# Kernel optimization log

Measured on AMD Instinct MI355X. Metric: run time of the kernel, lower is better.

## Reference

```python
import jax, jax.numpy as jnp
import numpy as np


def setup_inputs() -> dict:
    key = jax.random.key(0)
    k1, k2 = jax.random.split(key)
    B, D, S = 8, 64, 512
    x = jax.random.normal(k1, (B, D, S), dtype=jnp.float32)
    # bracket_products[0]: bias-free Linear(2*D -> D); stored as (2*D, D), applied feat @ W
    W = jax.random.normal(k2, (2 * D, D), dtype=jnp.float32) * (1.0 / np.sqrt(2 * D))
    return {"x": x, "W": W}


def reference(x, W):
    # x: (B, D, S); W: (2D, D)
    B, D, S = x.shape
    # torch builds y_out[b, :, i, j] = concat(x[b,:,j], x[b,:,i]) for i >= j (tril), zeros elsewhere,
    # then applies Linear(2D->D). Split W so the full linear is a broadcast sum of two per-position
    # projections, avoiding the explicit (B, 2D, S, S) scatter.
    W_w, W_h = W[:D], W[D:]                      # x_w part (col j), x_h part (row i)
    a = jnp.einsum('bdj,dk->bjk', x, W_w)        # (B, S, D): column-j contribution
    b = jnp.einsum('bdi,dk->bik', x, W_h)        # (B, S, D): row-i contribution
    mask = jnp.tril(jnp.ones((S, S), dtype=x.dtype))  # rows i >= cols j
    # pair[b,i,j,k] == bracket linear output at (row i, col j); zero on strict upper triangle
    pair = (a[:, None, :, :] + b[:, :, None, :]) * mask[None, :, :, None]  # (B, S, S, D)
    n = jnp.linalg.norm(pair, axis=-1)           # L2 over channel dim -> (B, S, S)
    wmat = 1.0 - n                                # upper triangle: 1 - 0 = 1, matching torch
    # torch: einsum('bdw,bdwi->bdi', x, weight) with weight (B,1,S,S) broadcast over d
    c = jnp.einsum('bdw,bwi->bdi', x, wmat)       # contract over row index w
    return c
```

## Files before the change

kernel.cpp:

```cpp
#include <hip/hip_runtime.h>
#include <hip/hip_bf16.h>
#include <math.h>

#define NB 8
#define ND 64
#define NS 512

typedef __attribute__((ext_vector_type(8))) short bf16x8;
typedef __attribute__((ext_vector_type(4))) float f32x4;
typedef __attribute__((ext_vector_type(4))) unsigned int u32x4;
typedef __attribute__((ext_vector_type(2))) unsigned int u32x2;

__device__ __forceinline__ unsigned int pk2(float lo, float hi) {
    __hip_bfloat162 h = __float22bfloat162_rn(make_float2(lo, hi));
    unsigned int u;
    __builtin_memcpy(&u, &h, 4);
    return u;
}
__device__ __forceinline__ unsigned short f2bf_s(float f) {
    __hip_bfloat16 h = __float2bfloat16(f);
    unsigned short u;
    __builtin_memcpy(&u, &h, 2);
    return u;
}

#define MFMA __builtin_amdgcn_mfma_f32_16x16x32_bf16

__global__ __launch_bounds__(256) void k_warm(const float* __restrict__ x,
                                              const float* __restrict__ W) {
    int idx = blockIdx.x * 256 + threadIdx.x;
    float4 v = ((const float4*)x)[idx];
    float s = v.x + v.y + v.z + v.w;
    if (idx < 2048) {
        float4 w4 = ((const float4*)W)[idx];
        s += w4.x + w4.y + w4.z + w4.w;
    }
    asm volatile("" :: "v"(s));
}

__global__ __launch_bounds__(256, 2) void k_part(const float* __restrict__ x,
                                                 const float* __restrict__ W,
                                                 float* __restrict__ part) {
    __shared__ __align__(16) unsigned short WT[128 * 64];
    __shared__ __align__(16) unsigned short xwd_i[64 * 64];
    __shared__ __align__(16) unsigned short xwd_u[64 * 64];
    __shared__ __align__(16) unsigned short xdw[64 * 64];
    __shared__ __align__(16) unsigned short alds[64 * 64];
    __shared__ __align__(16) unsigned short blds[64 * 64];
    __shared__ __align__(16) unsigned short wmb[64 * 64];
    __shared__ float na_lds[64], nb_lds[64];

    int b = blockIdx.y;
    int v = blockIdx.x;
    int u = 0;
    while ((u + 1) * (u + 2) / 2 <= v) ++u;
    int ti = v - u * (u + 1) / 2;
    int i0 = ti * 64, w0 = u * 64;

    int t = threadIdx.x;
    int lane = t & 63, wv = t >> 6, c = lane & 15, g = lane >> 4, c7 = c & 7;
    int wl = t & 63, w2 = t >> 6;

    float xi_[16], xu_[16];
#pragma unroll
    for (int j = 0; j < 2; ++j)
#pragma unroll
        for (int e = 0; e < 8; ++e) {
            int d = 8 * (2 * w2 + j) + e;
            const float* base = x + ((size_t)(b * ND) + d) * NS;
            xi_[8 * j + e] = base[i0 + wl];
            xu_[8 * j + e] = base[w0 + wl];
        }
    float4 xd_[4];
#pragma unroll
    for (int q = 0; q < 2; ++q) {
        int e = t + 256 * q;
        int d = e >> 3, wc = e & 7;
        const float4* p4 = (const float4*)(x + ((size_t)(b * ND) + d) * NS + w0 + 8 * wc);
        xd_[2 * q]     = p4[0];
        xd_[2 * q + 1] = p4[1];
    }
#pragma unroll
    for (int j = 0; j < 2; ++j) {
        int dblk = 2 * w2 + j;
        u32x4 hi, hu;
#pragma unroll
        for (int e = 0; e < 4; ++e) {
            hi[e] = pk2(xi_[8 * j + 2 * e], xi_[8 * j + 2 * e + 1]);
            hu[e] = pk2(xu_[8 * j + 2 * e], xu_[8 * j + 2 * e + 1]);
        }
        *(u32x4*)&xwd_i[wl * 64 + ((dblk ^ (wl & 7)) << 3)] = hi;
        *(u32x4*)&xwd_u[wl * 64 + ((dblk ^ (wl & 7)) << 3)] = hu;
    }
#pragma unroll
    for (int q = 0; q < 2; ++q) {
        int e = t + 256 * q;
        int d = e >> 3, wc = e & 7;
        float4 v0 = xd_[2 * q], v1 = xd_[2 * q + 1];
        u32x4 h;
        h[0] = pk2(v0.x, v0.y); h[1] = pk2(v0.z, v0.w);
        h[2] = pk2(v1.x, v1.y); h[3] = pk2(v1.z, v1.w);
        *(u32x4*)&xdw[d * 64 + ((wc ^ (d & 7)) << 3)] = h;
    }
    {
        int n = t & 127, half = t >> 7;
        float wv_[32];
#pragma unroll
        for (int p = 0; p < 4; ++p)
#pragma unroll
            for (int dd = 0; dd < 8; ++dd) {
                int dg = half * 4 + p;
                wv_[8 * p + dd] =
                    W[(size_t)(dg * 8 + dd) * ND + (n & 63) + ((n >> 6) * (ND * ND))];
            }
#pragma unroll
        for (int p = 0; p < 4; ++p) {
            int dg = half * 4 + p;
            u32x4 h;
#pragma unroll
            for (int dd = 0; dd < 4; ++dd)
                h[dd] = pk2(wv_[8 * p + 2 * dd], wv_[8 * p + 2 * dd + 1]);
            *(u32x4*)&WT[n * 64 + ((dg ^ (n & 7)) << 3)] = h;
        }
    }
    __syncthreads();

    {
        f32x4 aacc[4] = {{0,0,0,0},{0,0,0,0},{0,0,0,0},{0,0,0,0}};
        f32x4 bacc[4] = {{0,0,0,0},{0,0,0,0},{0,0,0,0},{0,0,0,0}};
#pragma unroll
        for (int ks = 0; ks < 2; ++ks) {
            int row = 16 * wv + c;
            bf16x8 Pi = *(const bf16x8*)&xwd_i[row * 64 + (((4 * ks + g) ^ c7) << 3)];
            bf16x8 Pu = *(const bf16x8*)&xwd_u[row * 64 + (((4 * ks + g) ^ c7) << 3)];
#pragma unroll
            for (int qb = 0; qb < 4; ++qb) {
                bf16x8 Qw = *(const bf16x8*)&WT[(16 * qb + c) * 64 + (((4 * ks + g) ^ c7) << 3)];
                bf16x8 Qh = *(const bf16x8*)&WT[(64 + 16 * qb + c) * 64 + (((4 * ks + g) ^ c7) << 3)];
                aacc[qb] = MFMA(Pi, Qw, aacc[qb], 0, 0, 0);
                bacc[qb] = MFMA(Pu, Qh, bacc[qb], 0, 0, 0);
            }
        }
#pragma unroll
        for (int r = 0; r < 4; ++r) {
            float sa = aacc[0][r] * aacc[0][r] + aacc[1][r] * aacc[1][r]
                     + aacc[2][r] * aacc[2][r] + aacc[3][r] * aacc[3][r];
            float sb = bacc[0][r] * bacc[0][r] + bacc[1][r] * bacc[1][r]
                     + bacc[2][r] * bacc[2][r] + bacc[3][r] * bacc[3][r];
            sa += __shfl_xor(sa, 1, 64); sa += __shfl_xor(sa, 2, 64);
            sa += __shfl_xor(sa, 4, 64); sa += __shfl_xor(sa, 8, 64);
            sb += __shfl_xor(sb, 1, 64); sb += __shfl_xor(sb, 2, 64);
            sb += __shfl_xor(sb, 4, 64); sb += __shfl_xor(sb, 8, 64);
            if (c == 0) {
                na_lds[16 * wv + 4 * g + r] = sa;
                nb_lds[16 * wv + 4 * g + r] = sb;
            }
        }
#pragma unroll
        for (int qb = 0; qb < 4; ++qb)
#pragma unroll
            for (int r = 0; r < 4; ++r) {
                int row = 16 * wv + 4 * g + r, k = 16 * qb + c;
                int off = row * 64 + (((k >> 3) ^ (row & 7)) << 3) + (k & 7);
                alds[off] = f2bf_s(aacc[qb][r]);
                blds[off] = f2bf_s(bacc[qb][r]);
            }
    }
    __syncthreads();

    {
        int wrow = 16 * wv + c;
        bf16x8 P0 = *(const bf16x8*)&blds[wrow * 64 + ((g ^ c7) << 3)];
        bf16x8 P1 = *(const bf16x8*)&blds[wrow * 64 + (((4 + g) ^ c7) << 3)];
        float nbv[4];
#pragma unroll
        for (int r = 0; r < 4; ++r) nbv[r] = nb_lds[16 * wv + 4 * g + r];
        int wbase = w0 + 16 * wv + 4 * g;
#pragma unroll
        for (int n = 0; n < 4; ++n) {
            int arow = 16 * n + c;
            f32x4 a1 = {0.f, 0.f, 0.f, 0.f};
            bf16x8 Q0 = *(const bf16x8*)&alds[arow * 64 + ((g ^ c7) << 3)];
            bf16x8 Q1 = *(const bf16x8*)&alds[arow * 64 + (((4 + g) ^ c7) << 3)];
            a1 = MFMA(P0, Q0, a1, 0, 0, 0);
            a1 = MFMA(P1, Q1, a1, 0, 0, 0);
            float navv = na_lds[arow];
            int i_glob = i0 + arow;
            float vals[4];
#pragma unroll
            for (int r = 0; r < 4; ++r) {
                float s2v = navv + nbv[r] + 2.f * a1[r];
                vals[r] = (i_glob <= wbase + r) ? -sqrtf(fmaxf(s2v, 0.f)) : 0.f;
            }
            u32x2 pk;
            pk[0] = pk2(vals[0], vals[1]);
            pk[1] = pk2(vals[2], vals[3]);
            int wblk = 2 * wv + (g >> 1);
            *(u32x2*)&wmb[arow * 64 + ((wblk ^ (arow & 7)) << 3) + 4 * (g & 1)] = pk;
        }
    }
    __syncthreads();

    {
        int il = 16 * wv + c;
        bf16x8 a20 = *(const bf16x8*)&wmb[il * 64 + ((g ^ c7) << 3)];
        bf16x8 a21 = *(const bf16x8*)&wmb[il * 64 + (((4 + g) ^ c7) << 3)];
#pragma unroll
        for (int nd = 0; nd < 4; ++nd) {
            int d = 16 * nd + c;
            bf16x8 q0 = *(const bf16x8*)&xdw[d * 64 + ((g ^ c7) << 3)];
            bf16x8 q1 = *(const bf16x8*)&xdw[d * 64 + (((4 + g) ^ c7) << 3)];
            f32x4 acc = {0.f, 0.f, 0.f, 0.f};
            acc = MFMA(a20, q0, acc, 0, 0, 0);
            acc = MFMA(a21, q1, acc, 0, 0, 0);
            float* pp = part + (((size_t)u * NB + b) * ND + d) * NS + i0 + 16 * wv + 4 * g;
            *(f32x4*)pp = acc;
        }
    }
}

__global__ __launch_bounds__(128) void k_red(const float* __restrict__ x,
                                             const float* __restrict__ part,
                                             float* __restrict__ out) {
    __shared__ float red[2];
    int b = blockIdx.y, d = blockIdx.x, t = threadIdx.x;
    const float* xr = x + ((size_t)b * ND + d) * NS;

    float4 xv = *(const float4*)(xr + 4 * t);
    float s = xv.x + xv.y + xv.z + xv.w;
#pragma unroll
    for (int m = 32; m >= 1; m >>= 1) s += __shfl_xor(s, m, 64);
    if ((t & 63) == 0) red[t >> 6] = s;
    __syncthreads();
    float rs = red[0] + red[1];

    int it = t >> 4;
    f32x4 vv = {rs, rs, rs, rs};
#pragma unroll
    for (int u = 0; u < 8; ++u) {
        if (u >= it) {
            f32x4 pv = *(const f32x4*)&part[(((size_t)u * NB + b) * ND + d) * NS + 4 * t];
            vv[0] += pv[0]; vv[1] += pv[1]; vv[2] += pv[2]; vv[3] += pv[3];
        }
    }
    *(f32x4*)&out[((size_t)b * ND + d) * NS + 4 * t] = vv;
}

extern "C" void kernel_launch(void* const* d_in, const int* in_sizes, int n_in,
                              void* d_out, int out_size, void* d_ws, size_t ws_size,
                              hipStream_t stream) {
    const float* x = (const float*)d_in[0];
    const float* W = (const float*)d_in[1];
    float* out  = (float*)d_out;
    float* part = (float*)d_ws;

    k_warm<<<dim3(256),    dim3(256), 0, stream>>>(x, W);
    k_part<<<dim3(36, NB), dim3(256), 0, stream>>>(x, W, part);
    k_red <<<dim3(ND, NB), dim3(128), 0, stream>>>(x, part, out);
}
```

Before: 22.19 us.

## Precompute per-position projections and norms in a prep kernel, drop redundant recompute

The tile kernel recomputed the a and b projections (x times W) for both its row and column blocks in every one of 36 tiles per batch. A separate prep kernel now computes each 64-position block's projections, squared norms and a bf16 copy of x once, writing them to the workspace. The pair kernel then just loads bf16 fragments directly from global memory into registers. The warm-up kernel is removed. This trades redundant MFMA work and W staging for extra global round-trips and one more kernel-launch dependency.

```diff
diff --git a/kernel.cpp b/kernel.cpp
--- a/kernel.cpp
+++ b/kernel.cpp
@@ -8,8 +8,8 @@
 
 typedef __attribute__((ext_vector_type(8))) short bf16x8;
 typedef __attribute__((ext_vector_type(4))) float f32x4;
+typedef __attribute__((ext_vector_type(4))) unsigned short us4;
 typedef __attribute__((ext_vector_type(4))) unsigned int u32x4;
-typedef __attribute__((ext_vector_type(2))) unsigned int u32x2;
 
 __device__ __forceinline__ unsigned int pk2(float lo, float hi) {
     __hip_bfloat162 h = __float22bfloat162_rn(make_float2(lo, hi));
@@ -26,29 +26,120 @@
 
 #define MFMA __builtin_amdgcn_mfma_f32_16x16x32_bf16
 
-__global__ __launch_bounds__(256) void k_warm(const float* __restrict__ x,
-                                              const float* __restrict__ W) {
-    int idx = blockIdx.x * 256 + threadIdx.x;
-    float4 v = ((const float4*)x)[idx];
-    float s = v.x + v.y + v.z + v.w;
-    if (idx < 2048) {
-        float4 w4 = ((const float4*)W)[idx];
-        s += w4.x + w4.y + w4.z + w4.w;
-    }
-    asm volatile("" :: "v"(s));
-}
-
-__global__ __launch_bounds__(256, 2) void k_part(const float* __restrict__ x,
-                                                 const float* __restrict__ W,
-                                                 float* __restrict__ part) {
+__global__ __launch_bounds__(256) void k_prep(const float* __restrict__ x,
+                                              const float* __restrict__ W,
+                                              unsigned short* __restrict__ a_bf,
+                                              unsigned short* __restrict__ b_bf,
+                                              float* __restrict__ na,
+                                              float* __restrict__ nb,
+                                              unsigned short* __restrict__ x_bf) {
+    __shared__ __align__(16) unsigned short xT[64 * 64];
     __shared__ __align__(16) unsigned short WT[128 * 64];
-    __shared__ __align__(16) unsigned short xwd_i[64 * 64];
-    __shared__ __align__(16) unsigned short xwd_u[64 * 64];
-    __shared__ __align__(16) unsigned short xdw[64 * 64];
-    __shared__ __align__(16) unsigned short alds[64 * 64];
-    __shared__ __align__(16) unsigned short blds[64 * 64];
-    __shared__ __align__(16) unsigned short wmb[64 * 64];
-    __shared__ float na_lds[64], nb_lds[64];
+
+    int b  = blockIdx.y;
+    int j0 = blockIdx.x * 64;
+    int t  = threadIdx.x;
+    int lane = t & 63, wv = t >> 6, c = lane & 15, g = lane >> 4, c7 = c & 7;
+    int wl = t & 63, w2 = t >> 6;
+
+    float xi_[16];
+#pragma unroll
+    for (int j = 0; j < 2; ++j)
+#pragma unroll
+        for (int e = 0; e < 8; ++e) {
+            int d = 8 * (2 * w2 + j) + e;
+            xi_[8 * j + e] = x[((size_t)(b * ND) + d) * NS + j0 + wl];
+        }
+#pragma unroll
+    for (int j = 0; j < 2; ++j) {
+        int dblk = 2 * w2 + j;
+        u32x4 h;
+#pragma unroll
+        for (int e = 0; e < 4; ++e)
+            h[e] = pk2(xi_[8 * j + 2 * e], xi_[8 * j + 2 * e + 1]);
+        *(u32x4*)&xT[wl * 64 + ((dblk ^ (wl & 7)) << 3)] = h;
+    }
+    {
+        int n = t & 127, half = t >> 7;
+        float wv_[32];
+#pragma unroll
+        for (int p = 0; p < 4; ++p)
+#pragma unroll
+            for (int dd = 0; dd < 8; ++dd) {
+                int dg = half * 4 + p;
+                wv_[8 * p + dd] =
+                    W[(size_t)(dg * 8 + dd) * ND + (n & 63) + ((n >> 6) * (ND * ND))];
+            }
+#pragma unroll
+        for (int p = 0; p < 4; ++p) {
+            int dg = half * 4 + p;
+            u32x4 h;
+#pragma unroll
+            for (int dd = 0; dd < 4; ++dd)
+                h[dd] = pk2(wv_[8 * p + 2 * dd], wv_[8 * p + 2 * dd + 1]);
+            *(u32x4*)&WT[n * 64 + ((dg ^ (n & 7)) << 3)] = h;
+        }
+    }
+#pragma unroll
+    for (int q = 0; q < 2; ++q) {
+        int e = t + 256 * q;
+        int d = e >> 3, wc = e & 7;
+        const float4* p4 = (const float4*)(x + ((size_t)(b * ND) + d) * NS + j0 + 8 * wc);
+        float4 v0 = p4[0], v1 = p4[1];
+        u32x4 h;
+        h[0] = pk2(v0.x, v0.y); h[1] = pk2(v0.z, v0.w);
+        h[2] = pk2(v1.x, v1.y); h[3] = pk2(v1.z, v1.w);
+        *(u32x4*)(x_bf + ((size_t)(b * ND) + d) * NS + j0 + 8 * wc) = h;
+    }
+    __syncthreads();
+
+    f32x4 aacc[4] = {{0,0,0,0},{0,0,0,0},{0,0,0,0},{0,0,0,0}};
+    f32x4 bacc[4] = {{0,0,0,0},{0,0,0,0},{0,0,0,0},{0,0,0,0}};
+#pragma unroll
+    for (int ks = 0; ks < 2; ++ks) {
+        int row = 16 * wv + c;
+        bf16x8 P = *(const bf16x8*)&xT[row * 64 + (((4 * ks + g) ^ c7) << 3)];
+#pragma unroll
+        for (int qb = 0; qb < 4; ++qb) {
+            bf16x8 Qw = *(const bf16x8*)&WT[(16 * qb + c) * 64 + (((4 * ks + g) ^ c7) << 3)];
+            bf16x8 Qh = *(const bf16x8*)&WT[(64 + 16 * qb + c) * 64 + (((4 * ks + g) ^ c7) << 3)];
+            aacc[qb] = MFMA(P, Qw, aacc[qb], 0, 0, 0);
+            bacc[qb] = MFMA(P, Qh, bacc[qb], 0, 0, 0);
+        }
+    }
+#pragma unroll
+    for (int r = 0; r < 4; ++r) {
+        float sa = aacc[0][r] * aacc[0][r] + aacc[1][r] * aacc[1][r]
+                 + aacc[2][r] * aacc[2][r] + aacc[3][r] * aacc[3][r];
+        float sb = bacc[0][r] * bacc[0][r] + bacc[1][r] * bacc[1][r]
+                 + bacc[2][r] * bacc[2][r] + bacc[3][r] * bacc[3][r];
+        sa += __shfl_xor(sa, 1, 64); sa += __shfl_xor(sa, 2, 64);
+        sa += __shfl_xor(sa, 4, 64); sa += __shfl_xor(sa, 8, 64);
+        sb += __shfl_xor(sb, 1, 64); sb += __shfl_xor(sb, 2, 64);
+        sb += __shfl_xor(sb, 4, 64); sb += __shfl_xor(sb, 8, 64);
+        if (c == 0) {
+            na[b * NS + j0 + 16 * wv + 4 * g + r] = sa;
+            nb[b * NS + j0 + 16 * wv + 4 * g + r] = sb;
+        }
+    }
+#pragma unroll
+    for (int qb = 0; qb < 4; ++qb)
+#pragma unroll
+        for (int r = 0; r < 4; ++r) {
+            int row = 16 * wv + 4 * g + r, k = 16 * qb + c;
+            size_t off = ((size_t)b * NS + j0 + row) * ND + k;
+            a_bf[off] = f2bf_s(aacc[qb][r]);
+            b_bf[off] = f2bf_s(bacc[qb][r]);
+        }
+}
+
+__global__ __launch_bounds__(256) void k_c(const unsigned short* __restrict__ x_bf,
+                                           const unsigned short* __restrict__ a_bf,
+                                           const unsigned short* __restrict__ b_bf,
+                                           const float* __restrict__ na,
+                                           const float* __restrict__ nb,
+                                           float* __restrict__ part) {
+    __shared__ unsigned short wm_lds[64 * 64];
 
     int b = blockIdx.y;
     int v = blockIdx.x;
@@ -58,164 +149,71 @@
     int i0 = ti * 64, w0 = u * 64;
 
     int t = threadIdx.x;
-    int lane = t & 63, wv = t >> 6, c = lane & 15, g = lane >> 4, c7 = c & 7;
-    int wl = t & 63, w2 = t >> 6;
-
-    float xi_[16], xu_[16];
-#pragma unroll
-    for (int j = 0; j < 2; ++j)
-#pragma unroll
-        for (int e = 0; e < 8; ++e) {
-            int d = 8 * (2 * w2 + j) + e;
-            const float* base = x + ((size_t)(b * ND) + d) * NS;
-            xi_[8 * j + e] = base[i0 + wl];
-            xu_[8 * j + e] = base[w0 + wl];
-        }
-    float4 xd_[4];
-#pragma unroll
-    for (int q = 0; q < 2; ++q) {
-        int e = t + 256 * q;
-        int d = e >> 3, wc = e & 7;
-        const float4* p4 = (const float4*)(x + ((size_t)(b * ND) + d) * NS + w0 + 8 * wc);
-        xd_[2 * q]     = p4[0];
-        xd_[2 * q + 1] = p4[1];
-    }
-#pragma unroll
-    for (int j = 0; j < 2; ++j) {
-        int dblk = 2 * w2 + j;
-        u32x4 hi, hu;
-#pragma unroll
-        for (int e = 0; e < 4; ++e) {
-            hi[e] = pk2(xi_[8 * j + 2 * e], xi_[8 * j + 2 * e + 1]);
-            hu[e] = pk2(xu_[8 * j + 2 * e], xu_[8 * j + 2 * e + 1]);
-        }
-        *(u32x4*)&xwd_i[wl * 64 + ((dblk ^ (wl & 7)) << 3)] = hi;
-        *(u32x4*)&xwd_u[wl * 64 + ((dblk ^ (wl & 7)) << 3)] = hu;
-    }
-#pragma unroll
-    for (int q = 0; q < 2; ++q) {
-        int e = t + 256 * q;
-        int d = e >> 3, wc = e & 7;
-        float4 v0 = xd_[2 * q], v1 = xd_[2 * q + 1];
-        u32x4 h;
-        h[0] = pk2(v0.x, v0.y); h[1] = pk2(v0.z, v0.w);
-        h[2] = pk2(v1.x, v1.y); h[3] = pk2(v1.z, v1.w);
-        *(u32x4*)&xdw[d * 64 + ((wc ^ (d & 7)) << 3)] = h;
-    }
+    int lane = t & 63, wv = t >> 6;
+    int c = lane & 15, g = lane >> 4;
+
+    bf16x8 afrag[2], bfrag[4][2], xfrag[4][2];
     {
-        int n = t & 127, half = t >> 7;
-        float wv_[32];
-#pragma unroll
-        for (int p = 0; p < 4; ++p)
-#pragma unroll
-            for (int dd = 0; dd < 8; ++dd) {
-                int dg = half * 4 + p;
-                wv_[8 * p + dd] =
-                    W[(size_t)(dg * 8 + dd) * ND + (n & 63) + ((n >> 6) * (ND * ND))];
-            }
-#pragma unroll
-        for (int p = 0; p < 4; ++p) {
-            int dg = half * 4 + p;
-            u32x4 h;
-#pragma unroll
-            for (int dd = 0; dd < 4; ++dd)
-                h[dd] = pk2(wv_[8 * p + 2 * dd], wv_[8 * p + 2 * dd + 1]);
-            *(u32x4*)&WT[n * 64 + ((dg ^ (n & 7)) << 3)] = h;
-        }
+        const unsigned short* bb = b_bf + ((size_t)(b * NS + w0 + 16 * wv + c)) * ND + g * 8;
+        afrag[0] = *(const bf16x8*)(bb);
+        afrag[1] = *(const bf16x8*)(bb + 32);
+    }
+#pragma unroll
+    for (int n = 0; n < 4; ++n) {
+        const unsigned short* aa = a_bf + ((size_t)(b * NS + i0 + 16 * n + c)) * ND + g * 8;
+        bfrag[n][0] = *(const bf16x8*)(aa);
+        bfrag[n][1] = *(const bf16x8*)(aa + 32);
+    }
+#pragma unroll
+    for (int nd = 0; nd < 4; ++nd) {
+        const unsigned short* xx = x_bf + ((size_t)(b * ND + 16 * nd + c)) * NS + w0 + 8 * g;
+        xfrag[nd][0] = *(const bf16x8*)(xx);
+        xfrag[nd][1] = *(const bf16x8*)(xx + 32);
+    }
+    float nbv[4], nav[4];
+#pragma unroll
+    for (int r = 0; r < 4; ++r) nbv[r] = nb[b * NS + w0 + 16 * wv + 4 * g + r];
+#pragma unroll
+    for (int n = 0; n < 4; ++n) nav[n] = na[b * NS + i0 + 16 * n + c];
+
+    int wbase = w0 + 16 * wv + 4 * g;
+#pragma unroll
+    for (int n = 0; n < 4; ++n) {
+        f32x4 acc = {0.f, 0.f, 0.f, 0.f};
+        acc = MFMA(afrag[0], bfrag[n][0], acc, 0, 0, 0);
+        acc = MFMA(afrag[1], bfrag[n][1], acc, 0, 0, 0);
+        int i_loc  = 16 * n + c;
+        int i_glob = i0 + i_loc;
+        float vals[4];
+#pragma unroll
+        for (int r = 0; r < 4; ++r) {
+            float s2 = nav[n] + nbv[r] + 2.f * acc[r];
+            vals[r] = (i_glob <= wbase + r) ? -sqrtf(fmaxf(s2, 0.f)) : 0.f;
+        }
+        us4 pk;
+        pk[0] = f2bf_s(vals[0]); pk[1] = f2bf_s(vals[1]);
+        pk[2] = f2bf_s(vals[2]); pk[3] = f2bf_s(vals[3]);
+        int wblk = 2 * wv + (g >> 1);
+        int hidx = i_loc * 64 + ((wblk ^ (i_loc & 7)) << 3) + 4 * (g & 1);
+        *(us4*)(&wm_lds[hidx]) = pk;
     }
     __syncthreads();
 
-    {
-        f32x4 aacc[4] = {{0,0,0,0},{0,0,0,0},{0,0,0,0},{0,0,0,0}};
-        f32x4 bacc[4] = {{0,0,0,0},{0,0,0,0},{0,0,0,0},{0,0,0,0}};
-#pragma unroll
-        for (int ks = 0; ks < 2; ++ks) {
-            int row = 16 * wv + c;
-            bf16x8 Pi = *(const bf16x8*)&xwd_i[row * 64 + (((4 * ks + g) ^ c7) << 3)];
-            bf16x8 Pu = *(const bf16x8*)&xwd_u[row * 64 + (((4 * ks + g) ^ c7) << 3)];
-#pragma unroll
-            for (int qb = 0; qb < 4; ++qb) {
-                bf16x8 Qw = *(const bf16x8*)&WT[(16 * qb + c) * 64 + (((4 * ks + g) ^ c7) << 3)];
-                bf16x8 Qh = *(const bf16x8*)&WT[(64 + 16 * qb + c) * 64 + (((4 * ks + g) ^ c7) << 3)];
-                aacc[qb] = MFMA(Pi, Qw, aacc[qb], 0, 0, 0);
-                bacc[qb] = MFMA(Pu, Qh, bacc[qb], 0, 0, 0);
-            }
-        }
-#pragma unroll
-        for (int r = 0; r < 4; ++r) {
-            float sa = aacc[0][r] * aacc[0][r] + aacc[1][r] * aacc[1][r]
-                     + aacc[2][r] * aacc[2][r] + aacc[3][r] * aacc[3][r];
-            float sb = bacc[0][r] * bacc[0][r] + bacc[1][r] * bacc[1][r]
-                     + bacc[2][r] * bacc[2][r] + bacc[3][r] * bacc[3][r];
-            sa += __shfl_xor(sa, 1, 64); sa += __shfl_xor(sa, 2, 64);
-            sa += __shfl_xor(sa, 4, 64); sa += __shfl_xor(sa, 8, 64);
-            sb += __shfl_xor(sb, 1, 64); sb += __shfl_xor(sb, 2, 64);
-            sb += __shfl_xor(sb, 4, 64); sb += __shfl_xor(sb, 8, 64);
-            if (c == 0) {
-                na_lds[16 * wv + 4 * g + r] = sa;
-                nb_lds[16 * wv + 4 * g + r] = sb;
-            }
-        }
-#pragma unroll
-        for (int qb = 0; qb < 4; ++qb)
-#pragma unroll
-            for (int r = 0; r < 4; ++r) {
-                int row = 16 * wv + 4 * g + r, k = 16 * qb + c;
-                int off = row * 64 + (((k >> 3) ^ (row & 7)) << 3) + (k & 7);
-                alds[off] = f2bf_s(aacc[qb][r]);
-                blds[off] = f2bf_s(bacc[qb][r]);
-            }
-    }
-    __syncthreads();
-
-    {
-        int wrow = 16 * wv + c;
-        bf16x8 P0 = *(const bf16x8*)&blds[wrow * 64 + ((g ^ c7) << 3)];
-        bf16x8 P1 = *(const bf16x8*)&blds[wrow * 64 + (((4 + g) ^ c7) << 3)];
-        float nbv[4];
-#pragma unroll
-        for (int r = 0; r < 4; ++r) nbv[r] = nb_lds[16 * wv + 4 * g + r];
-        int wbase = w0 + 16 * wv + 4 * g;
-#pragma unroll
-        for (int n = 0; n < 4; ++n) {
-            int arow = 16 * n + c;
-            f32x4 a1 = {0.f, 0.f, 0.f, 0.f};
-            bf16x8 Q0 = *(const bf16x8*)&alds[arow * 64 + ((g ^ c7) << 3)];
-            bf16x8 Q1 = *(const bf16x8*)&alds[arow * 64 + (((4 + g) ^ c7) << 3)];
-            a1 = MFMA(P0, Q0, a1, 0, 0, 0);
-            a1 = MFMA(P1, Q1, a1, 0, 0, 0);
-            float navv = na_lds[arow];
-            int i_glob = i0 + arow;
-            float vals[4];
-#pragma unroll
-            for (int r = 0; r < 4; ++r) {
-                float s2v = navv + nbv[r] + 2.f * a1[r];
-                vals[r] = (i_glob <= wbase + r) ? -sqrtf(fmaxf(s2v, 0.f)) : 0.f;
-            }
-            u32x2 pk;
-            pk[0] = pk2(vals[0], vals[1]);
-            pk[1] = pk2(vals[2], vals[3]);
-            int wblk = 2 * wv + (g >> 1);
-            *(u32x2*)&wmb[arow * 64 + ((wblk ^ (arow & 7)) << 3) + 4 * (g & 1)] = pk;
-        }
-    }
-    __syncthreads();
-
+    bf16x8 a2[2];
     {
         int il = 16 * wv + c;
-        bf16x8 a20 = *(const bf16x8*)&wmb[il * 64 + ((g ^ c7) << 3)];
-        bf16x8 a21 = *(const bf16x8*)&wmb[il * 64 + (((4 + g) ^ c7) << 3)];
-#pragma unroll
-        for (int nd = 0; nd < 4; ++nd) {
-            int d = 16 * nd + c;
-            bf16x8 q0 = *(const bf16x8*)&xdw[d * 64 + ((g ^ c7) << 3)];
-            bf16x8 q1 = *(const bf16x8*)&xdw[d * 64 + (((4 + g) ^ c7) << 3)];
-            f32x4 acc = {0.f, 0.f, 0.f, 0.f};
-            acc = MFMA(a20, q0, acc, 0, 0, 0);
-            acc = MFMA(a21, q1, acc, 0, 0, 0);
-            float* pp = part + (((size_t)u * NB + b) * ND + d) * NS + i0 + 16 * wv + 4 * g;
-            *(f32x4*)pp = acc;
-        }
+#pragma unroll
+        for (int s = 0; s < 2; ++s)
+            a2[s] = *(const bf16x8*)(&wm_lds[il * 64 + (((4 * s + g) ^ (il & 7)) << 3)]);
+    }
+#pragma unroll
+    for (int nd = 0; nd < 4; ++nd) {
+        f32x4 acc = {0.f, 0.f, 0.f, 0.f};
+        acc = MFMA(a2[0], xfrag[nd][0], acc, 0, 0, 0);
+        acc = MFMA(a2[1], xfrag[nd][1], acc, 0, 0, 0);
+        int d = 16 * nd + c;
+        float* pp = part + (((size_t)u * NB + b) * ND + d) * NS + i0 + 16 * wv + 4 * g;
+        *(f32x4*)pp = acc;
     }
 }
 
@@ -251,10 +249,16 @@
                               hipStream_t stream) {
     const float* x = (const float*)d_in[0];
     const float* W = (const float*)d_in[1];
-    float* out  = (float*)d_out;
-    float* part = (float*)d_ws;
-
-    k_warm<<<dim3(256),    dim3(256), 0, stream>>>(x, W);
-    k_part<<<dim3(36, NB), dim3(256), 0, stream>>>(x, W, part);
-    k_red <<<dim3(ND, NB), dim3(128), 0, stream>>>(x, part, out);
-}
+    float* out = (float*)d_out;
+
+    unsigned short* a_bf = (unsigned short*)d_ws;
+    unsigned short* b_bf = a_bf + (size_t)NB * NS * ND;
+    unsigned short* x_bf = b_bf + (size_t)NB * NS * ND;
+    float* na_p = (float*)(x_bf + (size_t)NB * NS * ND);
+    float* nb_p = na_p + NB * NS;
+    float* part = nb_p + NB * NS;
+
+    k_prep<<<dim3(NS / 64, NB), dim3(256), 0, stream>>>(x, W, a_bf, b_bf, na_p, nb_p, x_bf);
+    k_c   <<<dim3(36, NB),      dim3(256), 0, stream>>>(x_bf, a_bf, b_bf, na_p, nb_p, part);
+    k_red <<<dim3(ND, NB),      dim3(128), 0, stream>>>(x, part, out);
+}
```

Measured after the change: 23.39 us. +5.4%, slower.
